# Kernel tuning notes

Measured on AMD Instinct MI355X. Metric: run time of the kernel, lower is better.

The kernel has to match this reference:

```python
import jax, jax.numpy as jnp
import numpy as np

D_MODEL = 1024
NUM_HEADS = 16
B, S = 1, 4096


def setup_inputs() -> dict:
    key = jax.random.key(0)
    kx, kq, kk, kv, ko = jax.random.split(key, 5)
    std = (1.0 / D_MODEL) ** 0.5
    def trunc(k):
        return std * jax.random.truncated_normal(k, -3.0, 3.0, (D_MODEL, D_MODEL), dtype=jnp.float32)
    return {
        "x": jax.random.normal(kx, (B, S, D_MODEL), dtype=jnp.float32),
        "W_Q": trunc(kq),
        "W_K": trunc(kk),
        "W_V": trunc(kv),
        "W_O": trunc(ko),
    }


def reference(x, W_Q, W_K, W_V, W_O):
    Bx, Sx, Dm = x.shape
    H = NUM_HEADS
    d_attn = Dm // H
    # projections (torch code uses x @ W.T)
    Q = x @ W_Q.T
    K = x @ W_K.T
    V = x @ W_V.T
    # [B, H, S, d]
    Q = Q.reshape(Bx, Sx, H, d_attn).transpose(0, 2, 1, 3)
    K = K.reshape(Bx, Sx, H, d_attn).transpose(0, 2, 1, 3)
    V = V.reshape(Bx, Sx, H, d_attn).transpose(0, 2, 1, 3)
    scale = 1.0 / jnp.sqrt(jnp.asarray(d_attn, dtype=x.dtype))
    # [B, H, S, S] scores
    attn = jnp.einsum("bhqd,bhkd->bhqk", Q, K) * scale
    causal = jnp.tril(jnp.ones((Sx, Sx), dtype=bool))
    attn = jnp.where(causal, attn, jnp.asarray(-jnp.inf, dtype=attn.dtype))
    probs = jax.nn.softmax(attn, axis=-1)
    y = jnp.einsum("bhqk,bhkd->bhqd", probs, V)
    y = y.transpose(0, 2, 1, 3).reshape(Bx, Sx, Dm)
    return y @ W_O.T
```

## Files before the change

### kernel.cpp

```cpp
#include <hip/hip_runtime.h>

#define S_LEN 4096
#define DMODEL 1024
#define NHEADS 16

typedef __attribute__((ext_vector_type(8))) short bf16x8;
typedef __attribute__((ext_vector_type(4))) float f32x4;
typedef unsigned short u16;
typedef unsigned int u32;
typedef unsigned long long u64;

#define MEMFENCE asm volatile("" ::: "memory")

__device__ inline u16 f2bf(float f) {
    union { float f; u32 u; } v; v.f = f;
    u32 r = v.u + 0x7fffu + ((v.u >> 16) & 1u);
    return (u16)(r >> 16);
}

__device__ inline u32 pkbf2(float a, float b) {
    union { float f; u32 u; } ua, ub; ua.f = a; ub.f = b;
    const u32 ra = ua.u + 0x7fffu + ((ua.u >> 16) & 1u);
    const u32 rb = ub.u + 0x7fffu + ((ub.u >> 16) & 1u);
    return __builtin_amdgcn_perm(rb, ra, 0x07060302u);
}

__device__ inline u32 pkbf2f(float a, float b) {
    union { float f; u32 u; } ua, ub; ua.f = a; ub.f = b;
    const u32 ra = ua.u + 0x8000u;
    const u32 rb = ub.u + 0x8000u;
    return __builtin_amdgcn_perm(rb, ra, 0x07060302u);
}

__device__ inline void cp16(const void* g, void* l) {
    __builtin_amdgcn_global_load_lds(
        (const __attribute__((address_space(1))) unsigned int*)g,
        (__attribute__((address_space(3))) unsigned int*)l, 16, 0, 0);
}

__global__ __launch_bounds__(256) void cvt_all(const float* __restrict__ x,
                                               const float* __restrict__ wq,
                                               const float* __restrict__ wk,
                                               const float* __restrict__ wv,
                                               const float* __restrict__ wo,
                                               u16* __restrict__ xb,
                                               u16* __restrict__ w3,
                                               u16* __restrict__ wob) {
    const int b = blockIdx.x;
    const float* s; u16* d; int off;
    const int NW = DMODEL * DMODEL;
    if (b < 2048)      { s = x;  d = xb;          off = b * 2048; }
    else if (b < 2560) { s = wq; d = w3;          off = (b - 2048) * 2048; }
    else if (b < 3072) { s = wk; d = w3 + NW;     off = (b - 2560) * 2048; }
    else if (b < 3584) { s = wv; d = w3 + 2 * NW; off = (b - 3072) * 2048; }
    else               { s = wo; d = wob;         off = (b - 3584) * 2048; }
    const int i = off + threadIdx.x * 8;
    const float4 a = *(const float4*)(s + i);
    const float4 c = *(const float4*)(s + i + 4);
    u16 t[8];
    t[0] = f2bf(a.x); t[1] = f2bf(a.y); t[2] = f2bf(a.z); t[3] = f2bf(a.w);
    t[4] = f2bf(c.x); t[5] = f2bf(c.y); t[6] = f2bf(c.z); t[7] = f2bf(c.w);
    *(bf16x8*)(d + i) = *(const bf16x8*)t;
}

__global__ __launch_bounds__(256, 2) void gemm_qkv(const u16* __restrict__ A,
                                                   const u16* __restrict__ B3,
                                                   u16* __restrict__ Qo,
                                                   u16* __restrict__ Ko,
                                                   u16* __restrict__ Vo) {
    __shared__ __align__(16) u16 As[3][128 * 32];
    __shared__ __align__(16) u16 Bs[3][192 * 32];
    const int tid = threadIdx.x, lane = tid & 63, wave = tid >> 6;
    const int wm = (wave >> 1) * 64, wn = (wave & 1) * 96;
    const int m0 = blockIdx.y * 128, n0 = blockIdx.x * 192;
    const int l15 = lane & 15, quad = lane >> 4;

    f32x4 acc[4][6];
#pragma unroll
    for (int i = 0; i < 4; i++)
#pragma unroll
        for (int j = 0; j < 6; j++) acc[i][j] = (f32x4){0.f, 0.f, 0.f, 0.f};

    const int r0 = tid >> 2, c0 = (tid & 3) * 8;

#define STAGE_QKV(buf, kkb)                                                        \
    {                                                                              \
        cp16(A + (size_t)(m0 + r0) * 1024 + (kkb) + c0,        As[buf] + r0 * 32 + c0); \
        cp16(A + (size_t)(m0 + r0 + 64) * 1024 + (kkb) + c0,   As[buf] + (r0 + 64) * 32 + c0); \
        cp16(B3 + (size_t)(n0 + r0) * 1024 + (kkb) + c0,       Bs[buf] + r0 * 32 + c0); \
        cp16(B3 + (size_t)(n0 + r0 + 64) * 1024 + (kkb) + c0,  Bs[buf] + (r0 + 64) * 32 + c0); \
        cp16(B3 + (size_t)(n0 + r0 + 128) * 1024 + (kkb) + c0, Bs[buf] + (r0 + 128) * 32 + c0); \
    }

#define COMPUTE_QKV(cur)                                                           \
    {                                                                              \
        bf16x8 af[4], bfr[6];                                                      \
        _Pragma("unroll")                                                          \
        for (int i = 0; i < 4; i++)                                                \
            af[i] = *(const bf16x8*)(As[cur] + (wm + i * 16 + l15) * 32 + quad * 8); \
        _Pragma("unroll")                                                          \
        for (int j = 0; j < 6; j++)                                                \
            bfr[j] = *(const bf16x8*)(Bs[cur] + (wn + j * 16 + l15) * 32 + quad * 8); \
        _Pragma("unroll")                                                          \
        for (int i = 0; i < 4; i++)                                                \
            _Pragma("unroll")                                                      \
            for (int j = 0; j < 6; j++)                                            \
                acc[i][j] = __builtin_amdgcn_mfma_f32_16x16x32_bf16(af[i], bfr[j], acc[i][j], 0, 0, 0); \
    }

    STAGE_QKV(0, 0);
    MEMFENCE;
    STAGE_QKV(1, 32);
    MEMFENCE;

    for (int ks = 0; ks < 31; ks++) {
        asm volatile("s_waitcnt vmcnt(5)" ::: "memory");
        __builtin_amdgcn_s_barrier();
        __builtin_amdgcn_sched_barrier(0);
        if (ks < 30) {
            STAGE_QKV((ks + 2) % 3, (ks + 2) * 32);
            MEMFENCE;
        }
        COMPUTE_QKV(ks % 3);
    }
    asm volatile("s_waitcnt vmcnt(0)" ::: "memory");
    __builtin_amdgcn_s_barrier();
    __builtin_amdgcn_sched_barrier(0);
    COMPUTE_QKV(1);
#undef STAGE_QKV
#undef COMPUTE_QKV

    const int colbase = n0 + wn;
#pragma unroll
    for (int j = 0; j < 6; j++) {
        const int col = colbase + j * 16 + l15;
        const int which = col >> 10;
        const int cr = col & 1023;
        const int h = cr >> 6, c = cr & 63;
        u16* dst = (which == 0) ? Qo : (which == 1) ? Ko : Vo;
        u16* base = dst + (size_t)h * S_LEN * 64;
        if (which < 2) {
            const float sc = (which == 0) ? 0.125f * 1.4426950408889634f : 1.0f;
#pragma unroll
            for (int i = 0; i < 4; i++) {
#pragma unroll
                for (int r = 0; r < 4; r++) {
                    const int row = m0 + wm + i * 16 + quad * 4 + r;
                    base[(size_t)row * 64 + c] = f2bf(acc[i][j][r] * sc);
                }
            }
        } else {
#pragma unroll
            for (int i = 0; i < 4; i++) {
                const int row0 = m0 + wm + i * 16 + quad * 4;
                const u32 y0 = pkbf2(acc[i][j][0], acc[i][j][1]);
                const u32 y1 = pkbf2(acc[i][j][2], acc[i][j][3]);
                *(u64*)(base + (size_t)c * S_LEN + row0) = (u64)y0 | ((u64)y1 << 32);
            }
        }
    }
}

__global__ __launch_bounds__(256) void gemm_out(const u16* __restrict__ A,
                                                const u16* __restrict__ B,
                                                float* __restrict__ C) {
    __shared__ __align__(16) u16 As[2][64 * 64];
    __shared__ __align__(16) u16 Bs[2][128 * 64];
    const int tid = threadIdx.x, lane = tid & 63, wave = tid >> 6;
    const int wm = (wave >> 1) * 32, wn = (wave & 1) * 64;
    const int bx = blockIdx.x;
    const int n0 = (bx & 7) * 128, m0 = (bx >> 3) * 64;
    const int l15 = lane & 15, quad = lane >> 4;
    const int swz = l15 & 7;

    f32x4 acc[2][4];
#pragma unroll
    for (int i = 0; i < 2; i++)
#pragma unroll
        for (int j = 0; j < 4; j++) acc[i][j] = (f32x4){0.f, 0.f, 0.f, 0.f};

#define STAGE_OUT(buf, kb)                                                              \
    {                                                                                   \
        _Pragma("unroll")                                                               \
        for (int q = 0; q < 2; q++) {                                                   \
            const int ch = tid + q * 256;                                               \
            const int ar = ch >> 3, ac = ((ch & 7) ^ (ar & 7)) * 8;                     \
            cp16(A + (size_t)(m0 + ar) * 1024 + (kb) + ac, As[buf] + ch * 8);           \
        }                                                                               \
        _Pragma("unroll")                                                               \
        for (int q = 0; q < 4; q++) {                                                   \
            const int ch = tid + q * 256;                                               \
            const int br = ch >> 3, bc = ((ch & 7) ^ (br & 7)) * 8;                     \
            cp16(B + (size_t)(n0 + br) * 1024 + (kb) + bc, Bs[buf] + ch * 8);           \
        }                                                                               \
    }

    STAGE_OUT(0, 0);
    int cur = 0;
    for (int kk = 0; kk < 1024; kk += 64) {
        __syncthreads();
        if (kk + 64 < 1024) STAGE_OUT(cur ^ 1, kk + 64);
#pragma unroll
        for (int h = 0; h < 2; h++) {
            const int cc = (h * 4 + quad) ^ swz;
            bf16x8 af[2], bfr[4];
#pragma unroll
            for (int i = 0; i < 2; i++)
                af[i] = *(const bf16x8*)(As[cur] + (wm + i * 16 + l15) * 64 + cc * 8);
#pragma unroll
            for (int j = 0; j < 4; j++)
                bfr[j] = *(const bf16x8*)(Bs[cur] + (wn + j * 16 + l15) * 64 + cc * 8);
#pragma unroll
            for (int i = 0; i < 2; i++)
#pragma unroll
                for (int j = 0; j < 4; j++)
                    acc[i][j] = __builtin_amdgcn_mfma_f32_16x16x32_bf16(af[i], bfr[j], acc[i][j], 0, 0, 0);
        }
        cur ^= 1;
    }
#undef STAGE_OUT

#pragma unroll
    for (int i = 0; i < 2; i++)
#pragma unroll
        for (int j = 0; j < 4; j++)
#pragma unroll
            for (int r = 0; r < 4; r++) {
                const int row = m0 + wm + i * 16 + quad * 4 + r;
                const int col = n0 + wn + j * 16 + l15;
                C[(size_t)row * 1024 + col] = acc[i][j][r];
            }
}

__global__ __launch_bounds__(256, 3) void attn(const u16* __restrict__ Q,
                                               const u16* __restrict__ Kh,
                                               const u16* __restrict__ Vt,
                                               u16* __restrict__ Y) {
    __shared__ __align__(16) u16 KW[2][4][2048];
    __shared__ __align__(16) u16 VW[4][2048];
    const int b = blockIdx.x;
    const int head = b & 15;
    const int jq = 63 - (b >> 4);
    const int nkt = jq + 1;
    const int np = (nkt + 1) >> 1;
    const int qa = jq * 64;
    const int tid = threadIdx.x, lane = tid & 63, w = tid >> 6;
    const int l15 = lane & 15, quad = lane >> 4;
    const int swz = l15 & 7;

    const u16* Qp = Q + (size_t)head * S_LEN * 64;
    const u16* Kp = Kh + (size_t)head * S_LEN * 64;
    const u16* Vp = Vt + (size_t)head * 64 * S_LEN;

    bf16x8 qf[4][2];
#pragma unroll
    for (int qg = 0; qg < 4; qg++)
#pragma unroll
        for (int h = 0; h < 2; h++)
            qf[qg][h] = *(const bf16x8*)(Qp + (size_t)(qa + qg * 16 + l15) * 64 + h * 32 + quad * 8);
    MEMFENCE;

    f32x4 o[4][4];
#pragma unroll
    for (int dg = 0; dg < 4; dg++)
#pragma unroll
        for (int qg = 0; qg < 4; qg++) o[dg][qg] = (f32x4){0.f, 0.f, 0.f, 0.f};
    float lp[4] = {0.f, 0.f, 0.f, 0.f};

    const int keyl = w * 16 + quad * 4;
    const int s4 = (l15 >> 1) & 3;
    const int ceo = (((quad >> 1) ^ s4)) * 8 + (quad & 1) * 4;
    const int coo = ceo ^ 16;

    union PU { u32 d[4]; bf16x8 v; };
    union VU { u64 d[2]; bf16x8 v; };

#define STAGE_K(buf, kp2)                                                               \
    {                                                                                   \
        _Pragma("unroll")                                                               \
        for (int i = 0; i < 4; i++) {                                                   \
            const int gk = (kp2) * 128 + w * 16 + (i & 1) * 8 + (lane >> 3) + (i >> 1) * 64; \
            const int lc = (lane & 7) ^ (lane >> 3);                                    \
            cp16(Kp + (size_t)gk * 64 + lc * 8, KW[buf][w] + i * 512 + lane * 8);       \
        }                                                                               \
    }

#define STAGE_V(kp2)                                                                    \
    {                                                                                   \
        _Pragma("unroll")                                                               \
        for (int i = 0; i < 4; i++) {                                                   \
            const int d = i * 16 + (lane >> 2);                                         \
            const int L = (lane & 3) ^ ((lane >> 3) & 3);                               \
            const int s = (kp2) * 128 + w * 16 + (L >> 1) * 64 + (L & 1) * 8;           \
            cp16(Vp + (size_t)d * S_LEN + s, VW[w] + i * 512 + lane * 8);               \
        }                                                                               \
    }

#define QK_PHASE(DGE, DGO, HO)                                                          \
    {                                                                                   \
        const u16* Kb = KW[cur][w];                                                     \
        const bf16x8 kE0 = *(const bf16x8*)(Kb + l15 * 64 + (quad ^ swz) * 8);          \
        const bf16x8 kE1 = *(const bf16x8*)(Kb + l15 * 64 + ((4 ^ quad) ^ swz) * 8);    \
        const bf16x8 kO0 = *(const bf16x8*)(Kb + (16 + l15) * 64 + (quad ^ swz) * 8);   \
        const bf16x8 kO1 = *(const bf16x8*)(Kb + (16 + l15) * 64 + ((4 ^ quad) ^ swz) * 8); \
        __builtin_amdgcn_s_setprio(1);                                                  \
        _Pragma("unroll")                                                               \
        for (int qg = 0; qg < 4; qg++) {                                                \
            const int ql = qg * 16 + l15;                                               \
            f32x4 c = (f32x4){0.f, 0.f, 0.f, 0.f};                                      \
            c = __builtin_amdgcn_mfma_f32_16x16x32_bf16(kE0, qf[qg][0], c, 0, 0, 0);    \
            c = __builtin_amdgcn_mfma_f32_16x16x32_bf16(kE1, qf[qg][1], c, 0, 0, 0);    \
            float p0 = __builtin_amdgcn_exp2f(c[0]);                                    \
            float p1 = __builtin_amdgcn_exp2f(c[1]);                                    \
            float p2 = __builtin_amdgcn_exp2f(c[2]);                                    \
            float p3 = __builtin_amdgcn_exp2f(c[3]);                                    \
            if (DGE) {                                                                  \
                if (keyl + 0 > ql) p0 = 0.f;                                            \
                if (keyl + 1 > ql) p1 = 0.f;                                            \
                if (keyl + 2 > ql) p2 = 0.f;                                            \
                if (keyl + 3 > ql) p3 = 0.f;                                            \
            }                                                                           \
            lp[qg] += (p0 + p1) + (p2 + p3);                                            \
            pu[qg].d[0] = pkbf2f(p0, p1);                                               \
            pu[qg].d[1] = pkbf2f(p2, p3);                                               \
            if (HO) {                                                                   \
                f32x4 cc = (f32x4){0.f, 0.f, 0.f, 0.f};                                 \
                cc = __builtin_amdgcn_mfma_f32_16x16x32_bf16(kO0, qf[qg][0], cc, 0, 0, 0); \
                cc = __builtin_amdgcn_mfma_f32_16x16x32_bf16(kO1, qf[qg][1], cc, 0, 0, 0); \
                float q0 = __builtin_amdgcn_exp2f(cc[0]);                               \
                float q1 = __builtin_amdgcn_exp2f(cc[1]);                               \
                float q2 = __builtin_amdgcn_exp2f(cc[2]);                               \
                float q3 = __builtin_amdgcn_exp2f(cc[3]);                               \
                if (DGO) {                                                              \
                    if (keyl + 0 > ql) q0 = 0.f;                                        \
                    if (keyl + 1 > ql) q1 = 0.f;                                        \
                    if (keyl + 2 > ql) q2 = 0.f;                                        \
                    if (keyl + 3 > ql) q3 = 0.f;                                        \
                }                                                                       \
                lp[qg] += (q0 + q1) + (q2 + q3);                                        \
                pu[qg].d[2] = pkbf2f(q0, q1);                                           \
                pu[qg].d[3] = pkbf2f(q2, q3);                                           \
            } else {                                                                    \
                pu[qg].d[2] = 0u; pu[qg].d[3] = 0u;                                     \
            }                                                                           \
        }                                                                               \
        __builtin_amdgcn_s_setprio(0);                                                  \
    }

#define PV_PHASE()                                                                      \
    {                                                                                   \
        __builtin_amdgcn_s_setprio(1);                                                  \
        _Pragma("unroll")                                                               \
        for (int dg = 0; dg < 4; dg++) {                                                \
            const u16* vb = VW[w] + (dg * 16 + l15) * 32;                               \
            VU vf;                                                                      \
            vf.d[0] = *(const u64*)(vb + ceo);                                          \
            vf.d[1] = *(const u64*)(vb + coo);                                          \
            _Pragma("unroll")                                                           \
            for (int qg = 0; qg < 4; qg++)                                              \
                o[dg][qg] = __builtin_amdgcn_mfma_f32_16x16x32_bf16(vf.v, pu[qg].v, o[dg][qg], 0, 0, 0); \
        }                                                                               \
        __builtin_amdgcn_s_setprio(0);                                                  \
    }

    STAGE_K(0, 0);
    MEMFENCE;
    STAGE_V(0);
    MEMFENCE;

    int cur = 0;
    for (int kp = 0; kp < np - 1; kp++) {
        STAGE_K(cur ^ 1, kp + 1);
        asm volatile("s_waitcnt vmcnt(8)" ::: "memory");
        __builtin_amdgcn_sched_barrier(0);
        PU pu[4];
        QK_PHASE(false, false, true);
        asm volatile("s_waitcnt vmcnt(4)" ::: "memory");
        __builtin_amdgcn_sched_barrier(0);
        PV_PHASE();
        MEMFENCE;
        STAGE_V(kp + 1);
        MEMFENCE;
        cur ^= 1;
    }
    {
        asm volatile("s_waitcnt vmcnt(4)" ::: "memory");
        __builtin_amdgcn_sched_barrier(0);
        const bool dE = !(jq & 1);
        const bool hO = (jq & 1);
        PU pu[4];
        QK_PHASE(dE, true, hO);
        asm volatile("s_waitcnt vmcnt(0)" ::: "memory");
        __builtin_amdgcn_sched_barrier(0);
        PV_PHASE();
    }
#undef STAGE_K
#undef STAGE_V
#undef QK_PHASE
#undef PV_PHASE

    float* OR = (float*)&KW[0][0][0];
    float* LR = (float*)((char*)&KW[0][0][0] + 24576);
#pragma unroll
    for (int qg = 0; qg < 4; qg++) {
        lp[qg] += __shfl_xor(lp[qg], 16);
        lp[qg] += __shfl_xor(lp[qg], 32);
    }
    __syncthreads();
    if (lane < 16) {
#pragma unroll
        for (int qg = 0; qg < 4; qg++) LR[(w * 4 + qg) * 16 + lane] = lp[qg];
    }
    const int qrow = tid >> 2;
    const int qgr = qrow >> 4, lq = qrow & 15;
    const int dpart = (tid & 3) * 4;
    __syncthreads();
    const float lsum = LR[qgr * 16 + lq] + LR[(4 + qgr) * 16 + lq] +
                       LR[(8 + qgr) * 16 + lq] + LR[(12 + qgr) * 16 + lq];
    const float inv = 1.f / lsum;
#pragma unroll
    for (int dg = 0; dg < 4; dg++) {
        if (dg) __syncthreads();
#pragma unroll
        for (int qg = 0; qg < 4; qg++)
            *(f32x4*)&OR[((w * 4 + qg) * 16 + l15) * 20 + quad * 4] = o[dg][qg];
        __syncthreads();
        f32x4 s = (f32x4){0.f, 0.f, 0.f, 0.f};
#pragma unroll
        for (int sw = 0; sw < 4; sw++)
            s += *(const f32x4*)&OR[((sw * 4 + qgr) * 16 + lq) * 20 + dpart];
        const u32 y0 = pkbf2(s[0] * inv, s[1] * inv);
        const u32 y1 = pkbf2(s[2] * inv, s[3] * inv);
        *(u64*)(Y + (size_t)(qa + qrow) * DMODEL + head * 64 + dg * 16 + dpart) =
            (u64)y0 | ((u64)y1 << 32);
    }
}

extern "C" void kernel_launch(void* const* d_in, const int* in_sizes, int n_in,
                              void* d_out, int out_size, void* d_ws, size_t ws_size,
                              hipStream_t stream) {
    const float* x  = (const float*)d_in[0];
    const float* wq = (const float*)d_in[1];
    const float* wk = (const float*)d_in[2];
    const float* wv = (const float*)d_in[3];
    const float* wo = (const float*)d_in[4];
    float* out = (float*)d_out;

    u16* qh  = (u16*)d_ws;
    u16* kh  = qh + (size_t)S_LEN * DMODEL;
    u16* vt  = kh + (size_t)S_LEN * DMODEL;
    u16* xb  = vt + (size_t)S_LEN * DMODEL;
    u16* y   = xb;
    u16* wb3 = xb + (size_t)S_LEN * DMODEL;
    u16* wob = wb3 + (size_t)3 * DMODEL * DMODEL;

    const dim3 blk(256);

    cvt_all<<<4096, blk, 0, stream>>>(x, wq, wk, wv, wo, xb, wb3, wob);
    gemm_qkv<<<dim3(3 * DMODEL / 192, S_LEN / 128), blk, 0, stream>>>(xb, wb3, qh, kh, vt);
    attn<<<1024, blk, 0, stream>>>(qh, kh, vt, y);
    gemm_out<<<512, blk, 0, stream>>>(y, wob, out);
}
```

Baseline: 190.6 us.

## Single-buffer K tile in LDS and raise attention occupancy to five blocks

```diff
diff --git a/kernel.cpp b/kernel.cpp
--- a/kernel.cpp
+++ b/kernel.cpp
@@ -232,12 +232,11 @@
             }
 }
 
-__global__ __launch_bounds__(256, 3) void attn(const u16* __restrict__ Q,
+__global__ __launch_bounds__(256, 5) void attn(const u16* __restrict__ Q,
                                                const u16* __restrict__ Kh,
                                                const u16* __restrict__ Vt,
                                                u16* __restrict__ Y) {
-    __shared__ __align__(16) u16 KW[2][4][2048];
-    __shared__ __align__(16) u16 VW[4][2048];
+    __shared__ __align__(16) u16 SH[16384];
     const int b = blockIdx.x;
     const int head = b & 15;
     const int jq = 63 - (b >> 4);
@@ -248,6 +247,9 @@
     const int l15 = lane & 15, quad = lane >> 4;
     const int swz = l15 & 7;
 
+    u16* KB = SH + w * 2048;
+    u16* VB = SH + 8192 + w * 2048;
+
     const u16* Qp = Q + (size_t)head * S_LEN * 64;
     const u16* Kp = Kh + (size_t)head * S_LEN * 64;
     const u16* Vp = Vt + (size_t)head * 64 * S_LEN;
@@ -275,13 +277,13 @@
     union PU { u32 d[4]; bf16x8 v; };
     union VU { u64 d[2]; bf16x8 v; };
 
-#define STAGE_K(buf, kp2)                                                               \
+#define STAGE_K(kp2)                                                                    \
     {                                                                                   \
         _Pragma("unroll")                                                               \
         for (int i = 0; i < 4; i++) {                                                   \
             const int gk = (kp2) * 128 + w * 16 + (i & 1) * 8 + (lane >> 3) + (i >> 1) * 64; \
             const int lc = (lane & 7) ^ (lane >> 3);                                    \
-            cp16(Kp + (size_t)gk * 64 + lc * 8, KW[buf][w] + i * 512 + lane * 8);       \
+            cp16(Kp + (size_t)gk * 64 + lc * 8, KB + i * 512 + lane * 8);               \
         }                                                                               \
     }
 
@@ -292,24 +294,27 @@
             const int d = i * 16 + (lane >> 2);                                         \
             const int L = (lane & 3) ^ ((lane >> 3) & 3);                               \
             const int s = (kp2) * 128 + w * 16 + (L >> 1) * 64 + (L & 1) * 8;           \
-            cp16(Vp + (size_t)d * S_LEN + s, VW[w] + i * 512 + lane * 8);               \
-        }                                                                               \
-    }
-
-#define QK_PHASE(DGE, DGO, HO)                                                          \
+            cp16(Vp + (size_t)d * S_LEN + s, VB + i * 512 + lane * 8);                  \
+        }                                                                               \
+    }
+
+#define LOADK(KE0, KE1, KO0, KO1)                                                       \
+    KE0 = *(const bf16x8*)(KB + l15 * 64 + (quad ^ swz) * 8);                           \
+    KE1 = *(const bf16x8*)(KB + l15 * 64 + ((4 ^ quad) ^ swz) * 8);                     \
+    KO0 = *(const bf16x8*)(KB + (16 + l15) * 64 + (quad ^ swz) * 8);                    \
+    KO1 = *(const bf16x8*)(KB + (16 + l15) * 64 + ((4 ^ quad) ^ swz) * 8);              \
+    asm volatile("s_waitcnt lgkmcnt(0)" ::: "memory");                                  \
+    __builtin_amdgcn_sched_barrier(0);
+
+#define QK_PHASE(KE0, KE1, KO0, KO1, DGE, DGO, HO)                                      \
     {                                                                                   \
-        const u16* Kb = KW[cur][w];                                                     \
-        const bf16x8 kE0 = *(const bf16x8*)(Kb + l15 * 64 + (quad ^ swz) * 8);          \
-        const bf16x8 kE1 = *(const bf16x8*)(Kb + l15 * 64 + ((4 ^ quad) ^ swz) * 8);    \
-        const bf16x8 kO0 = *(const bf16x8*)(Kb + (16 + l15) * 64 + (quad ^ swz) * 8);   \
-        const bf16x8 kO1 = *(const bf16x8*)(Kb + (16 + l15) * 64 + ((4 ^ quad) ^ swz) * 8); \
         __builtin_amdgcn_s_setprio(1);                                                  \
         _Pragma("unroll")                                                               \
         for (int qg = 0; qg < 4; qg++) {                                                \
             const int ql = qg * 16 + l15;                                               \
             f32x4 c = (f32x4){0.f, 0.f, 0.f, 0.f};                                      \
-            c = __builtin_amdgcn_mfma_f32_16x16x32_bf16(kE0, qf[qg][0], c, 0, 0, 0);    \
-            c = __builtin_amdgcn_mfma_f32_16x16x32_bf16(kE1, qf[qg][1], c, 0, 0, 0);    \
+            c = __builtin_amdgcn_mfma_f32_16x16x32_bf16(KE0, qf[qg][0], c, 0, 0, 0);    \
+            c = __builtin_amdgcn_mfma_f32_16x16x32_bf16(KE1, qf[qg][1], c, 0, 0, 0);    \
             float p0 = __builtin_amdgcn_exp2f(c[0]);                                    \
             float p1 = __builtin_amdgcn_exp2f(c[1]);                                    \
             float p2 = __builtin_amdgcn_exp2f(c[2]);                                    \
@@ -325,8 +330,8 @@
             pu[qg].d[1] = pkbf2f(p2, p3);                                               \
             if (HO) {                                                                   \
                 f32x4 cc = (f32x4){0.f, 0.f, 0.f, 0.f};                                 \
-                cc = __builtin_amdgcn_mfma_f32_16x16x32_bf16(kO0, qf[qg][0], cc, 0, 0, 0); \
-                cc = __builtin_amdgcn_mfma_f32_16x16x32_bf16(kO1, qf[qg][1], cc, 0, 0, 0); \
+                cc = __builtin_amdgcn_mfma_f32_16x16x32_bf16(KO0, qf[qg][0], cc, 0, 0, 0); \
+                cc = __builtin_amdgcn_mfma_f32_16x16x32_bf16(KO1, qf[qg][1], cc, 0, 0, 0); \
                 float q0 = __builtin_amdgcn_exp2f(cc[0]);                               \
                 float q1 = __builtin_amdgcn_exp2f(cc[1]);                               \
                 float q2 = __builtin_amdgcn_exp2f(cc[2]);                               \
@@ -352,7 +357,7 @@
         __builtin_amdgcn_s_setprio(1);                                                  \
         _Pragma("unroll")                                                               \
         for (int dg = 0; dg < 4; dg++) {                                                \
-            const u16* vb = VW[w] + (dg * 16 + l15) * 32;                               \
+            const u16* vb = VB + (dg * 16 + l15) * 32;                                  \
             VU vf;                                                                      \
             vf.d[0] = *(const u64*)(vb + ceo);                                          \
             vf.d[1] = *(const u64*)(vb + coo);                                          \
@@ -363,44 +368,48 @@
         __builtin_amdgcn_s_setprio(0);                                                  \
     }
 
-    STAGE_K(0, 0);
+    STAGE_K(0);
     MEMFENCE;
     STAGE_V(0);
     MEMFENCE;
 
-    int cur = 0;
     for (int kp = 0; kp < np - 1; kp++) {
-        STAGE_K(cur ^ 1, kp + 1);
-        asm volatile("s_waitcnt vmcnt(8)" ::: "memory");
+        asm volatile("s_waitcnt vmcnt(4)" ::: "memory");
         __builtin_amdgcn_sched_barrier(0);
+        bf16x8 kE0, kE1, kO0, kO1;
+        LOADK(kE0, kE1, kO0, kO1);
+        STAGE_K(kp + 1);
+        MEMFENCE;
         PU pu[4];
-        QK_PHASE(false, false, true);
+        QK_PHASE(kE0, kE1, kO0, kO1, false, false, true);
         asm volatile("s_waitcnt vmcnt(4)" ::: "memory");
         __builtin_amdgcn_sched_barrier(0);
         PV_PHASE();
         MEMFENCE;
         STAGE_V(kp + 1);
         MEMFENCE;
-        cur ^= 1;
     }
     {
         asm volatile("s_waitcnt vmcnt(4)" ::: "memory");
         __builtin_amdgcn_sched_barrier(0);
+        bf16x8 kE0, kE1, kO0, kO1;
+        LOADK(kE0, kE1, kO0, kO1);
         const bool dE = !(jq & 1);
         const bool hO = (jq & 1);
         PU pu[4];
-        QK_PHASE(dE, true, hO);
+        QK_PHASE(kE0, kE1, kO0, kO1, dE, true, hO);
         asm volatile("s_waitcnt vmcnt(0)" ::: "memory");
         __builtin_amdgcn_sched_barrier(0);
         PV_PHASE();
     }
 #undef STAGE_K
 #undef STAGE_V
+#undef LOADK
 #undef QK_PHASE
 #undef PV_PHASE
 
-    float* OR = (float*)&KW[0][0][0];
-    float* LR = (float*)((char*)&KW[0][0][0] + 24576);
+    float* OR = (float*)&SH[0];
+    float* LR = (float*)((char*)&SH[0] + 24576);
 #pragma unroll
     for (int qg = 0; qg < 4; qg++) {
         lp[qg] += __shfl_xor(lp[qg], 16);
```

Result: slower. 435.1 us (+128.2%).
